# Optimization experiments

Measured on AMD Instinct MI355X. Metric: run time of the kernel, lower is better.

The kernel has to match this reference:

```python
import jax, jax.numpy as jnp
import numpy as np

NEG_SLOPE = 0.2  # PyG GATConv default negative_slope
BN_EPS = 1e-5


def gat_layer(x, src, dst, W, b, a_src, a_dst, heads, out_ch, concat):
    # x: [N, Fin]; W: [Fin, heads*out_ch]; a_src/a_dst: [heads, out_ch]
    N = x.shape[0]
    h = (x @ W).reshape(N, heads, out_ch)
    s = (h * a_src).sum(-1)            # [N, H]
    d = (h * a_dst).sum(-1)            # [N, H]
    e = jax.nn.leaky_relu(s[src] + d[dst], NEG_SLOPE)   # [E, H]
    # segment softmax over incoming edges of each destination node
    m = jax.ops.segment_max(e, dst, num_segments=N)
    ex = jnp.exp(e - m[dst])
    denom = jax.ops.segment_sum(ex, dst, num_segments=N)
    alpha = ex / (denom[dst] + 1e-16)                   # [E, H]
    out = jax.ops.segment_sum(alpha[:, :, None] * h[src], dst, num_segments=N)  # [N,H,C]
    out = out.reshape(N, heads * out_ch) if concat else out.mean(axis=1)
    return out + b


def batchnorm(x, gamma, beta):
    mu = x.mean(axis=0)
    var = x.var(axis=0)
    return gamma * (x - mu) * jax.lax.rsqrt(var + BN_EPS) + beta


def setup_inputs() -> dict:
    key = jax.random.key(0)
    ks = jax.random.split(key, 24)
    N, E, Fin, Hd, heads, C = 50000, 800000, 128, 64, 4, 2
    wdim = Hd * heads  # 256
    inp = {
        'x': jax.random.normal(ks[0], (N, Fin), jnp.float32),
        'edge_index': jax.random.randint(ks[1], (2, E), 0, N, jnp.int64),
    }
    def glorot(k, shape):
        fan = shape[0] + shape[-1]
        return jax.random.normal(k, shape, jnp.float32) * np.sqrt(2.0 / fan)
    # layer 0: Fin -> heads x Hd (concat)
    inp['W0'] = glorot(ks[2], (Fin, wdim)); inp['b0'] = jnp.zeros((wdim,), jnp.float32)
    inp['asrc0'] = glorot(ks[3], (heads, Hd)); inp['adst0'] = glorot(ks[4], (heads, Hd))
    inp['g0'] = jnp.ones((wdim,), jnp.float32); inp['be0'] = jnp.zeros((wdim,), jnp.float32)
    # layer 1: wdim -> heads x Hd (concat)
    inp['W1'] = glorot(ks[5], (wdim, wdim)); inp['b1'] = jnp.zeros((wdim,), jnp.float32)
    inp['asrc1'] = glorot(ks[6], (heads, Hd)); inp['adst1'] = glorot(ks[7], (heads, Hd))
    inp['g1'] = jnp.ones((wdim,), jnp.float32); inp['be1'] = jnp.zeros((wdim,), jnp.float32)
    # layer 2: wdim -> 1 head x Hd (no concat)
    inp['W2'] = glorot(ks[8], (wdim, Hd)); inp['b2'] = jnp.zeros((Hd,), jnp.float32)
    inp['asrc2'] = glorot(ks[9], (1, Hd)); inp['adst2'] = glorot(ks[10], (1, Hd))
    inp['g2'] = jnp.ones((Hd,), jnp.float32); inp['be2'] = jnp.zeros((Hd,), jnp.float32)
    # classifier: Linear(2*Hd, Hd) -> ReLU -> Linear(Hd, C)
    inp['Wc1'] = glorot(ks[11], (2 * Hd, Hd)); inp['bc1'] = jnp.zeros((Hd,), jnp.float32)
    inp['Wc2'] = glorot(ks[12], (Hd, C)); inp['bc2'] = jnp.zeros((C,), jnp.float32)
    return inp


def reference(x, edge_index, W0, b0, asrc0, adst0, g0, be0,
              W1, b1, asrc1, adst1, g1, be1,
              W2, b2, asrc2, adst2, g2, be2,
              Wc1, bc1, Wc2, bc2):
    N = x.shape[0]
    # add self-loops (PyG GATConv default)
    loops = jnp.arange(N, dtype=edge_index.dtype)
    src = jnp.concatenate([edge_index[0], loops])
    dst = jnp.concatenate([edge_index[1], loops])
    heads, Hd = asrc0.shape[0], asrc0.shape[1]

    h = gat_layer(x, src, dst, W0, b0, asrc0, adst0, heads, Hd, True)
    h = jax.nn.relu(batchnorm(h, g0, be0))
    h = gat_layer(h, src, dst, W1, b1, asrc1, adst1, heads, Hd, True)
    h = jax.nn.relu(batchnorm(h, g1, be1))
    h = gat_layer(h, src, dst, W2, b2, asrc2, adst2, 1, Hd, False)
    h = jax.nn.relu(batchnorm(h, g2, be2))

    pooled = jnp.concatenate([h.mean(axis=0, keepdims=True),
                              h.max(axis=0, keepdims=True)], axis=1)  # [1, 2*Hd]
    z = jax.nn.relu(pooled @ Wc1 + bc1)
    return z @ Wc2 + bc2  # [1, num_classes]
```

## Files before the change

### kernel.cpp

```cpp
#include <hip/hip_runtime.h>


typedef unsigned int uint;
typedef unsigned short ushort;

#define NEG_SLOPE 0.2f
#define BN_EPS 1e-5f
#define NB_RED 256

typedef __attribute__((ext_vector_type(2))) float f32x2;

__device__ __forceinline__ float bf2f(uint u) { return __uint_as_float(u << 16); }
__device__ __forceinline__ ushort f2bf(float f) {
    uint u = __float_as_uint(f);
    u += 0x7fff + ((u >> 16) & 1);
    return (ushort)(u >> 16);
}


__global__ void prep_kernel(const float* __restrict__ x, ushort* __restrict__ xb,
                            int total_real, int total_pad,
                            const float* __restrict__ W0, ushort* __restrict__ w0t,
                            const float* __restrict__ W1, ushort* __restrict__ w1t,
                            const float* __restrict__ W2, ushort* __restrict__ w2t,
                            const int* __restrict__ ei, int* __restrict__ deg, int E) {
    int i = blockIdx.x * blockDim.x + threadIdx.x;
    if (i < total_pad) {
        xb[i] = (i < total_real) ? f2bf(x[i]) : (ushort)0;
        return;
    }
    int j = i - total_pad;
    if (j < 32768) {
        int n = j / 128, k = j - n * 128;
        w0t[j] = f2bf(W0[(size_t)k * 256 + n]);
        return;
    }
    j -= 32768;
    if (j < 65536) {
        int n = j / 256, k = j - n * 256;
        w1t[j] = f2bf(W1[(size_t)k * 256 + n]);
        return;
    }
    j -= 65536;
    if (j < 16384) {
        int n = j / 256, k = j - n * 256;
        w2t[j] = f2bf(W2[(size_t)k * 64 + n]);
        return;
    }
    j -= 16384;
    if (j < E) atomicAdd(&deg[ei[E + j]], 1);
}


__global__ void scan_part(const int* __restrict__ deg, int* __restrict__ offsets,
                          int* __restrict__ bsum, int N) {
    __shared__ int sh[256];
    int t = threadIdx.x;
    int base = blockIdx.x * 1024 + t * 4;
    int v0 = (base + 0 < N) ? deg[base + 0] : 0;
    int v1 = (base + 1 < N) ? deg[base + 1] : 0;
    int v2 = (base + 2 < N) ? deg[base + 2] : 0;
    int v3 = (base + 3 < N) ? deg[base + 3] : 0;
    int s = v0 + v1 + v2 + v3;
    sh[t] = s;
    __syncthreads();
    for (int off = 1; off < 256; off <<= 1) {
        int y = (t >= off) ? sh[t - off] : 0;
        __syncthreads();
        sh[t] += y;
        __syncthreads();
    }
    int p = sh[t] - s;
    if (base + 0 < N) offsets[base + 0] = p;
    p += v0;
    if (base + 1 < N) offsets[base + 1] = p;
    p += v1;
    if (base + 2 < N) offsets[base + 2] = p;
    p += v2;
    if (base + 3 < N) offsets[base + 3] = p;
    if (t == 255) bsum[blockIdx.x] = sh[255];
}

__global__ void scan_top(const int* __restrict__ bsum, int* __restrict__ bexcl,
                         int nb, int* __restrict__ offsets, int N) {
    if (threadIdx.x == 0) {
        int run = 0;
        for (int b = 0; b < nb; ++b) { bexcl[b] = run; run += bsum[b]; }
        offsets[N] = run;
    }
}

__global__ void scan_add(int* __restrict__ offsets, int* __restrict__ cursor,
                         const int* __restrict__ bexcl, int N) {
    int add = bexcl[blockIdx.x];
    int base = blockIdx.x * 1024 + threadIdx.x * 4;
#pragma unroll
    for (int k = 0; k < 4; ++k) {
        int i = base + k;
        if (i < N) { int v = offsets[i] + add; offsets[i] = v; cursor[i] = v; }
    }
}

__global__ void scatter_kernel(const int* __restrict__ ei, int* __restrict__ cursor,
                               int* __restrict__ srcs, int E) {
    int e = blockIdx.x * blockDim.x + threadIdx.x;
    if (e < E) {
        int s = ei[e];
        int d = ei[E + e];
        int p = atomicAdd(&cursor[d], 1);
        srcs[p] = s;
    }
}


typedef __attribute__((ext_vector_type(8))) short bf16x8;
typedef __attribute__((ext_vector_type(4))) float floatx4;

template <int BN, int H>
__launch_bounds__(256)
__global__ void mfma_gemm_bt(const ushort* __restrict__ A, const ushort* __restrict__ Bt,
                             ushort* __restrict__ C, const float* __restrict__ asrc,
                             const float* __restrict__ adst, float* __restrict__ sv,
                             float* __restrict__ dv, int K, int Nn, int Mpad) {
    constexpr int WCOLS = (BN == 128) ? 2 : 1;
    constexpr int WROWS = 4 / WCOLS;
    constexpr int MT = 128 / (WROWS * 16);
    constexpr int NT = BN / (WCOLS * 16);
    constexpr int BCALLS = (BN * 32 * 2) / 4096;
    constexpr int SCH = (BN == 64) ? 8 : 32;
    constexpr int SSH = (BN == 64) ? 3 : 5;

    __shared__ ushort As[128 * 32];
    __shared__ ushort Bs[BN * 32];

    int t = threadIdx.x;
    int w = t >> 6, l = t & 63;

    int rb, cb;
    if (BN == 128) {
        int nbr = (int)gridDim.x >> 1;
        int full = (nbr & ~7) << 1;
        int id = blockIdx.x;
        if (id < full) {
            rb = ((id >> 4) << 3) + (id & 7);
            cb = (id >> 3) & 1;
        } else {
            int o = id - full;
            int rem = nbr & 7;
            rb = (nbr & ~7) + (rem ? (o % rem) : 0);
            cb = rem ? (o / rem) : 0;
        }
    } else {
        rb = blockIdx.x;
        cb = 0;
    }
    int row0 = rb * 128;
    int col0 = cb * BN;
    int wr = (w / WCOLS) * (MT * 16);
    int wc = (w % WCOLS) * (NT * 16);

    floatx4 acc[MT][NT];
#pragma unroll
    for (int mi = 0; mi < MT; ++mi)
#pragma unroll
        for (int ni = 0; ni < NT; ++ni)
#pragma unroll
            for (int r = 0; r < 4; ++r) acc[mi][ni][r] = 0.f;

    int mrow = l & 15;
    int kc = (l >> 4) * 8;

    for (int kt = 0; kt < K; kt += 32) {
#pragma unroll
        for (int c = 0; c < 2; ++c) {
            int idx = c * 256 + t;
            const ushort* gp = A + (size_t)(row0 + (idx >> 2)) * K + kt + (idx & 3) * 8;
            __builtin_amdgcn_global_load_lds(
                (const __attribute__((address_space(1))) void*)gp,
                (__attribute__((address_space(3))) void*)(As + (idx & ~63) * 8),
                16, 0, 0);
        }
#pragma unroll
        for (int c = 0; c < BCALLS; ++c) {
            int idx = c * 256 + t;
            const ushort* gp = Bt + (size_t)(col0 + (idx >> 2)) * K + kt + (idx & 3) * 8;
            __builtin_amdgcn_global_load_lds(
                (const __attribute__((address_space(1))) void*)gp,
                (__attribute__((address_space(3))) void*)(Bs + (idx & ~63) * 8),
                16, 0, 0);
        }
        __syncthreads();

        bf16x8 af[MT], bfr[NT];
#pragma unroll
        for (int mi = 0; mi < MT; ++mi)
            af[mi] = *(const bf16x8*)&As[(wr + mi * 16 + mrow) * 32 + kc];
#pragma unroll
        for (int ni = 0; ni < NT; ++ni)
            bfr[ni] = *(const bf16x8*)&Bs[(wc + ni * 16 + mrow) * 32 + kc];
#pragma unroll
        for (int mi = 0; mi < MT; ++mi)
#pragma unroll
            for (int ni = 0; ni < NT; ++ni)
                acc[mi][ni] = __builtin_amdgcn_mfma_f32_16x16x32_bf16(
                    af[mi], bfr[ni], acc[mi][ni], 0, 0, 0);
        __syncthreads();
    }

#pragma unroll
    for (int mi = 0; mi < MT; ++mi) {
        int rbase = row0 + wr + mi * 16 + (l >> 4) * 4;
#pragma unroll
        for (int ni = 0; ni < NT; ++ni) {
            int col = col0 + wc + ni * 16 + (l & 15);
            size_t sb = ((size_t)(col >> SSH) * Mpad) * SCH + (col & (SCH - 1));
#pragma unroll
            for (int r = 0; r < 4; ++r)
                C[sb + (size_t)(rbase + r) * SCH] = f2bf(acc[mi][ni][r]);
        }
    }

    float av[NT], bv[NT];
#pragma unroll
    for (int ni = 0; ni < NT; ++ni) {
        int ch = col0 + wc + ni * 16 + (l & 15);
        av[ni] = asrc[ch];
        bv[ni] = adst[ch];
    }
    int gh = (col0 + wc) >> 6;
#pragma unroll
    for (int mi = 0; mi < MT; ++mi) {
#pragma unroll
        for (int r = 0; r < 4; ++r) {
            float s = 0.f, d = 0.f;
#pragma unroll
            for (int ni = 0; ni < NT; ++ni) {
                float hv = acc[mi][ni][r];
                s += hv * av[ni];
                d += hv * bv[ni];
            }
#pragma unroll
            for (int m = 8; m >= 1; m >>= 1) {
                s += __shfl_xor(s, m);
                d += __shfl_xor(d, m);
            }
            if ((l & 15) == 0) {
                int row = row0 + wr + mi * 16 + (l >> 4) * 4 + r;
                sv[row * H + gh] = s;
                dv[row * H + gh] = d;
            }
        }
    }
}


#define CAP4 64

#define ACCUMW4(qv_, wt_) { \
    f32x2 wv_ = {(wt_), (wt_)}; \
    uint pr_[4] = {(qv_).x, (qv_).y, (qv_).z, (qv_).w}; \
    _Pragma("unroll") \
    for (int k_ = 0; k_ < 4; ++k_) { \
        f32x2 hv_ = {__uint_as_float(pr_[k_] << 16), \
                     __uint_as_float(pr_[k_] & 0xffff0000u)}; \
        ax[k_] += wv_ * hv_; \
    } }

#define LDQ4(kk_, wv_, qv_) { \
    int kq_ = (kk_); \
    if (kq_ < scnt) { \
        int nq_ = sidx[sub][kq_]; \
        wv_ = swgt[sub][kq_]; \
        qv_ = *(const uint4*)(gbase + (size_t)nq_ * 32); \
    } else { wv_ = 0.f; qv_.x = 0; qv_.y = 0; qv_.z = 0; qv_.w = 0; } }

__launch_bounds__(128)
__global__ void agg4_kernel(const ushort* __restrict__ hbT, const float* __restrict__ sv,
                            const float* __restrict__ dv, const int* __restrict__ offsets,
                            const int* __restrict__ srcs, const float* __restrict__ bias,
                            ushort* __restrict__ zb, int N, int Mpad) {
    __shared__ int   sidx[8][CAP4];
    __shared__ float swgt[8][CAP4];

    int t = threadIdx.x;
    int sub = t >> 4, gl = t & 15;
    int bid = blockIdx.x;
    int c = bid & 7;
    int head = c >> 1;
    int i = (bid >> 3) * 8 + sub;
    bool valid = i < N;

    int beg = 0, cnt = 0;
    if (valid) { beg = offsets[i]; cnt = offsets[i + 1] - beg; }
    int scnt = cnt < CAP4 ? cnt : CAP4;

    for (int k = gl; k < scnt; k += 16) sidx[sub][k] = srcs[beg + k];
    __syncthreads();

    float dvh = valid ? dv[i * 4 + head] : 0.f;
    float den = 0.f;
    for (int k = gl; k < scnt; k += 16) {
        float e = sv[sidx[sub][k] * 4 + head] + dvh;
        float wgt = __expf(fminf(fmaxf(e, NEG_SLOPE * e), 60.f));
        swgt[sub][k] = wgt;
        den += wgt;
    }
    den += __shfl_xor(den, 1);
    den += __shfl_xor(den, 2);
    den += __shfl_xor(den, 4);
    den += __shfl_xor(den, 8);
    __syncthreads();

    f32x2 ax[4] = {};
    int chunk = gl & 3;
    int esub = gl >> 2;
    const ushort* gbase = hbT + (size_t)c * Mpad * 32 + chunk * 8;

    float wA, wB;
    uint4 qA, qB;
    LDQ4(esub, wA, qA);
    LDQ4(esub + 4, wB, qB);
    for (int k = esub; k < scnt; k += 8) {
        float v0 = wA, v1 = wB;
        uint4 p0 = qA, p1 = qB;
        LDQ4(k + 8, wA, qA);
        LDQ4(k + 12, wB, qB);
        ACCUMW4(p0, v0);
        ACCUMW4(p1, v1);
    }

    if (cnt > CAP4) {
        float dslow = 0.f;
        for (int k2 = CAP4 + esub; k2 < cnt; k2 += 4) {
            int n = srcs[beg + k2];
            float e = sv[n * 4 + head] + dvh;
            float wgt = __expf(fminf(fmaxf(e, NEG_SLOPE * e), 60.f));
            if (chunk == 0) dslow += wgt;
            uint4 q4 = *(const uint4*)(gbase + (size_t)n * 32);
            ACCUMW4(q4, wgt);
        }
        dslow += __shfl_xor(dslow, 1);
        dslow += __shfl_xor(dslow, 2);
        dslow += __shfl_xor(dslow, 4);
        dslow += __shfl_xor(dslow, 8);
        den += dslow;
    }

#pragma unroll
    for (int j = 0; j < 4; ++j) {
        ax[j].x += __shfl_xor(ax[j].x, 4);
        ax[j].y += __shfl_xor(ax[j].y, 4);
        ax[j].x += __shfl_xor(ax[j].x, 8);
        ax[j].y += __shfl_xor(ax[j].y, 8);
    }

    if (valid && esub == 0) {
        float e_self = sv[i * 4 + head] + dvh;
        float wself = __expf(fminf(fmaxf(e_self, NEG_SLOPE * e_self), 60.f));
        uint4 qs = *(const uint4*)(gbase + (size_t)i * 32);
        ACCUMW4(qs, wself);
        float rden = 1.f / (den + wself + 1e-16f);
        const float* bb = bias + c * 32 + chunk * 8;
        uint4 o;
        o.x = (uint)f2bf(ax[0].x * rden + bb[0]) | ((uint)f2bf(ax[0].y * rden + bb[1]) << 16);
        o.y = (uint)f2bf(ax[1].x * rden + bb[2]) | ((uint)f2bf(ax[1].y * rden + bb[3]) << 16);
        o.z = (uint)f2bf(ax[2].x * rden + bb[4]) | ((uint)f2bf(ax[2].y * rden + bb[5]) << 16);
        o.w = (uint)f2bf(ax[3].x * rden + bb[6]) | ((uint)f2bf(ax[3].y * rden + bb[7]) << 16);
        *(uint4*)&zb[(size_t)i * 256 + c * 32 + chunk * 8] = o;
    }
}


__launch_bounds__(64)
__global__ void agg1_kernel(const ushort* __restrict__ hbT, const float* __restrict__ sv,
                            const float* __restrict__ dv, const int* __restrict__ offsets,
                            const int* __restrict__ srcs, const float* __restrict__ bias,
                            ushort* __restrict__ zb, int N, int Mpad) {
    int t = threadIdx.x;
    int sub = t >> 3, gl = t & 7;
    int bid = blockIdx.x;
    int c = bid & 7;
    int i = (bid >> 3) * 8 + sub;
    bool valid = i < N;

    int beg = 0, cnt = 0;
    if (valid) { beg = offsets[i]; cnt = offsets[i + 1] - beg; }

    float d_i = valid ? dv[i] : 0.f;
    const ushort* gbase = hbT + (size_t)c * Mpad * 8;

    f32x2 ax[4] = {};
    float den = 0.f;

    int k = gl;
    int nA = (k < cnt) ? srcs[beg + k] : 0;
    while (k < cnt) {
        int kn = k + 8;
        int nB = (kn < cnt) ? srcs[beg + kn] : 0;
        float s = sv[nA];
        uint4 q = *(const uint4*)(gbase + (size_t)nA * 8);
        float e = s + d_i;
        float wgt = __expf(fminf(fmaxf(e, NEG_SLOPE * e), 60.f));
        den += wgt;
        ACCUMW4(q, wgt);
        k = kn; nA = nB;
    }

    den += __shfl_xor(den, 1);
    den += __shfl_xor(den, 2);
    den += __shfl_xor(den, 4);
#pragma unroll
    for (int j = 0; j < 4; ++j) {
        ax[j].x += __shfl_xor(ax[j].x, 1);
        ax[j].y += __shfl_xor(ax[j].y, 1);
        ax[j].x += __shfl_xor(ax[j].x, 2);
        ax[j].y += __shfl_xor(ax[j].y, 2);
        ax[j].x += __shfl_xor(ax[j].x, 4);
        ax[j].y += __shfl_xor(ax[j].y, 4);
    }

    if (valid && gl == 0) {
        float e_self = sv[i] + d_i;
        float wself = __expf(fminf(fmaxf(e_self, NEG_SLOPE * e_self), 60.f));
        uint4 qs = *(const uint4*)(gbase + (size_t)i * 8);
        ACCUMW4(qs, wself);
        float rden = 1.f / (den + wself + 1e-16f);
        const float* bb = bias + c * 8;
        uint4 o;
        o.x = (uint)f2bf(ax[0].x * rden + bb[0]) | ((uint)f2bf(ax[0].y * rden + bb[1]) << 16);
        o.y = (uint)f2bf(ax[1].x * rden + bb[2]) | ((uint)f2bf(ax[1].y * rden + bb[3]) << 16);
        o.z = (uint)f2bf(ax[2].x * rden + bb[4]) | ((uint)f2bf(ax[2].y * rden + bb[5]) << 16);
        o.w = (uint)f2bf(ax[3].x * rden + bb[6]) | ((uint)f2bf(ax[3].y * rden + bb[7]) << 16);
        *(uint4*)&zb[(size_t)i * 64 + c * 8] = o;
    }
}


template <int F>
__launch_bounds__(256)
__global__ void bn_stats_kernel(const ushort* __restrict__ x, float* __restrict__ ps,
                                float* __restrict__ pq, int N) {
    constexpr int OCT = F / 8;
    __shared__ float lds_s[F], lds_q[F];
    int t = threadIdx.x;
    if (t < F) { lds_s[t] = 0.f; lds_q[t] = 0.f; }
    __syncthreads();

    float s[8] = {}, q[8] = {};
    int total8 = N * F / 8;
    for (int idx = blockIdx.x * 256 + t; idx < total8; idx += NB_RED * 256) {
        uint4 v = ((const uint4*)x)[idx];
        uint pr[4] = {v.x, v.y, v.z, v.w};
#pragma unroll
        for (int k = 0; k < 4; ++k) {
            float a = bf2f(pr[k] & 0xffffu);
            float b = bf2f(pr[k] >> 16);
            s[2 * k] += a;     q[2 * k] += a * a;
            s[2 * k + 1] += b; q[2 * k + 1] += b * b;
        }
    }
    int co = t % OCT;
#pragma unroll
    for (int j = 0; j < 8; ++j) {
        atomicAdd(&lds_s[co * 8 + j], s[j]);
        atomicAdd(&lds_q[co * 8 + j], q[j]);
    }
    __syncthreads();
    if (t < F) {
        ps[blockIdx.x * F + t] = lds_s[t];
        pq[blockIdx.x * F + t] = lds_q[t];
    }
}

__global__ void bn_final_kernel(const float* __restrict__ ps, const float* __restrict__ pq,
                                const float* __restrict__ g, const float* __restrict__ be,
                                float* __restrict__ scale, float* __restrict__ shift,
                                int N, int F) {
    int t = threadIdx.x;
    if (t < F) {
        float s = 0.f, q = 0.f;
        for (int b = 0; b < NB_RED; ++b) { s += ps[b * F + t]; q += pq[b * F + t]; }
        float mean = s / (float)N;
        float var = q / (float)N - mean * mean;
        float sc = g[t] * rsqrtf(var + BN_EPS);
        scale[t] = sc;
        shift[t] = be[t] - sc * mean;
    }
}

__global__ void bn_apply_kernel(uint* __restrict__ x, const float* __restrict__ scale,
                                const float* __restrict__ shift, int totalPairs, int Fmask) {
    int i = blockIdx.x * blockDim.x + threadIdx.x;
    if (i < totalPairs) {
        uint p = x[i];
        int c0 = (2 * i) & Fmask;
        float v0 = fmaxf(bf2f(p & 0xffffu) * scale[c0] + shift[c0], 0.f);
        float v1 = fmaxf(bf2f(p >> 16) * scale[c0 + 1] + shift[c0 + 1], 0.f);
        x[i] = (uint)f2bf(v0) | ((uint)f2bf(v1) << 16);
    }
}


__launch_bounds__(256)
__global__ void pool_kernel(const ushort* __restrict__ y, const float* __restrict__ scale,
                            const float* __restrict__ shift, float* __restrict__ psum,
                            float* __restrict__ pmax, int N) {
    constexpr int F = 64, OCT = 8;
    __shared__ float lds_s[F];
    __shared__ uint lds_m[F];
    int t = threadIdx.x;
    if (t < F) { lds_s[t] = 0.f; lds_m[t] = 0u; }
    __syncthreads();

    int co = t % OCT;
    float sc[8], sh[8];
#pragma unroll
    for (int j = 0; j < 8; ++j) { sc[j] = scale[co * 8 + j]; sh[j] = shift[co * 8 + j]; }

    float s[8] = {}, m[8] = {};
    int total8 = N * F / 8;
    for (int idx = blockIdx.x * 256 + t; idx < total8; idx += NB_RED * 256) {
        uint4 v = ((const uint4*)y)[idx];
        uint pr[4] = {v.x, v.y, v.z, v.w};
#pragma unroll
        for (int k = 0; k < 4; ++k) {
            float a = fmaxf(bf2f(pr[k] & 0xffffu) * sc[2 * k] + sh[2 * k], 0.f);
            float b = fmaxf(bf2f(pr[k] >> 16) * sc[2 * k + 1] + sh[2 * k + 1], 0.f);
            s[2 * k] += a;     m[2 * k] = fmaxf(m[2 * k], a);
            s[2 * k + 1] += b; m[2 * k + 1] = fmaxf(m[2 * k + 1], b);
        }
    }
#pragma unroll
    for (int j = 0; j < 8; ++j) {
        atomicAdd(&lds_s[co * 8 + j], s[j]);
        atomicMax(&lds_m[co * 8 + j], __float_as_uint(m[j]));
    }
    __syncthreads();
    if (t < F) {
        psum[blockIdx.x * F + t] = lds_s[t];
        pmax[blockIdx.x * F + t] = __uint_as_float(lds_m[t]);
    }
}

__global__ void classify_kernel(const float* __restrict__ psum, const float* __restrict__ pmax,
                                const float* __restrict__ Wc1, const float* __restrict__ bc1,
                                const float* __restrict__ Wc2, const float* __restrict__ bc2,
                                float* __restrict__ out, int N) {
    __shared__ float pooled[128];
    __shared__ float z[64];
    int t = threadIdx.x;
    if (t < 64) {
        float s = 0.f;
        for (int b = 0; b < NB_RED; ++b) s += psum[b * 64 + t];
        pooled[t] = s / (float)N;
    } else {
        int c = t - 64;
        float m = 0.f;
        for (int b = 0; b < NB_RED; ++b) m = fmaxf(m, pmax[b * 64 + c]);
        pooled[t] = m;
    }
    __syncthreads();
    if (t < 64) {
        float a = bc1[t];
        for (int k = 0; k < 128; ++k) a += pooled[k] * Wc1[k * 64 + t];
        z[t] = a > 0.f ? a : 0.f;
    }
    __syncthreads();
    if (t < 2) {
        float a = bc2[t];
        for (int j = 0; j < 64; ++j) a += z[j] * Wc2[j * 2 + t];
        out[t] = a;
    }
}


extern "C" void kernel_launch(void* const* d_in, const int* in_sizes, int n_in,
                              void* d_out, int out_size, void* d_ws, size_t ws_size,
                              hipStream_t stream) {
    const float* x   = (const float*)d_in[0];
    const int*   ei  = (const int*)d_in[1];
    const float* W0  = (const float*)d_in[2];  const float* b0  = (const float*)d_in[3];
    const float* as0 = (const float*)d_in[4];  const float* ad0 = (const float*)d_in[5];
    const float* g0  = (const float*)d_in[6];  const float* be0 = (const float*)d_in[7];
    const float* W1  = (const float*)d_in[8];  const float* b1  = (const float*)d_in[9];
    const float* as1 = (const float*)d_in[10]; const float* ad1 = (const float*)d_in[11];
    const float* g1  = (const float*)d_in[12]; const float* be1 = (const float*)d_in[13];
    const float* W2  = (const float*)d_in[14]; const float* b2  = (const float*)d_in[15];
    const float* as2 = (const float*)d_in[16]; const float* ad2 = (const float*)d_in[17];
    const float* g2  = (const float*)d_in[18]; const float* be2 = (const float*)d_in[19];
    const float* Wc1 = (const float*)d_in[20]; const float* bc1 = (const float*)d_in[21];
    const float* Wc2 = (const float*)d_in[22]; const float* bc2 = (const float*)d_in[23];
    float* out = (float*)d_out;

    const int N = in_sizes[0] / 128;
    const int E = in_sizes[1] / 2;
    const int Mpad = ((N + 127) / 128) * 128;
    const int NB_SCAN = (N + 1023) / 1024;
    const int NBROW = Mpad / 128;
    const int NB_AGG = ((N + 7) / 8) * 8;

    char* ws = (char*)d_ws;
    size_t o = 0;
    auto alloc = [&](size_t bytes) -> void* {
        void* p = ws + o;
        o = (o + bytes + 255) & ~(size_t)255;
        return p;
    };
    int*    deg     = (int*)alloc((size_t)N * 4);
    int*    offsets = (int*)alloc((size_t)(N + 1) * 4);
    int*    cursor  = (int*)alloc((size_t)N * 4);
    int*    srcs    = (int*)alloc((size_t)E * 4);
    int*    bsum    = (int*)alloc((size_t)NB_SCAN * 4);
    int*    bexcl   = (int*)alloc((size_t)NB_SCAN * 4);
    ushort* xb      = (ushort*)alloc((size_t)Mpad * 128 * 2);
    ushort* w0t     = (ushort*)alloc((size_t)256 * 128 * 2);
    ushort* w1t     = (ushort*)alloc((size_t)256 * 256 * 2);
    ushort* w2t     = (ushort*)alloc((size_t)64 * 256 * 2);
    ushort* hb      = (ushort*)alloc((size_t)Mpad * 256 * 2);
    ushort* zb      = (ushort*)alloc((size_t)Mpad * 256 * 2);
    float*  sv      = (float*)alloc((size_t)Mpad * 4 * 4);
    float*  dv      = (float*)alloc((size_t)Mpad * 4 * 4);
    float*  ps      = (float*)alloc((size_t)NB_RED * 256 * 4);
    float*  pq      = (float*)alloc((size_t)NB_RED * 256 * 4);
    float*  scale   = (float*)alloc(256 * 4);
    float*  shift   = (float*)alloc(256 * 4);
    float*  psum    = (float*)alloc((size_t)NB_RED * 64 * 4);
    float*  pmax    = (float*)alloc((size_t)NB_RED * 64 * 4);

    (void)hipMemsetAsync(deg, 0, (size_t)N * 4, stream);
    int prep_total = Mpad * 128 + 32768 + 65536 + 16384 + E;
    prep_kernel<<<(prep_total + 255) / 256, 256, 0, stream>>>(
        x, xb, N * 128, Mpad * 128, W0, w0t, W1, w1t, W2, w2t, ei, deg, E);

    scan_part<<<NB_SCAN, 256, 0, stream>>>(deg, offsets, bsum, N);
    scan_top<<<1, 64, 0, stream>>>(bsum, bexcl, NB_SCAN, offsets, N);
    scan_add<<<NB_SCAN, 256, 0, stream>>>(offsets, cursor, bexcl, N);
    scatter_kernel<<<(E + 255) / 256, 256, 0, stream>>>(ei, cursor, srcs, E);

    {
        mfma_gemm_bt<128, 4><<<NBROW * 2, 256, 0, stream>>>(xb, w0t, hb, as0, ad0, sv, dv,
                                                            128, 256, Mpad);
        agg4_kernel<<<NB_AGG, 128, 0, stream>>>(hb, sv, dv, offsets, srcs, b0, zb, N, Mpad);
        bn_stats_kernel<256><<<NB_RED, 256, 0, stream>>>(zb, ps, pq, N);
        bn_final_kernel<<<1, 256, 0, stream>>>(ps, pq, g0, be0, scale, shift, N, 256);
        bn_apply_kernel<<<(N * 128 + 255) / 256, 256, 0, stream>>>((uint*)zb, scale, shift,
                                                                   N * 128, 255);
    }
    {
        mfma_gemm_bt<128, 4><<<NBROW * 2, 256, 0, stream>>>(zb, w1t, hb, as1, ad1, sv, dv,
                                                            256, 256, Mpad);
        agg4_kernel<<<NB_AGG, 128, 0, stream>>>(hb, sv, dv, offsets, srcs, b1, zb, N, Mpad);
        bn_stats_kernel<256><<<NB_RED, 256, 0, stream>>>(zb, ps, pq, N);
        bn_final_kernel<<<1, 256, 0, stream>>>(ps, pq, g1, be1, scale, shift, N, 256);
        bn_apply_kernel<<<(N * 128 + 255) / 256, 256, 0, stream>>>((uint*)zb, scale, shift,
                                                                   N * 128, 255);
    }
    {
        mfma_gemm_bt<64, 1><<<NBROW, 256, 0, stream>>>(zb, w2t, hb, as2, ad2, sv, dv,
                                                       256, 64, Mpad);
        agg1_kernel<<<NB_AGG, 64, 0, stream>>>(hb, sv, dv, offsets, srcs, b2, zb, N, Mpad);
        bn_stats_kernel<64><<<NB_RED, 256, 0, stream>>>(zb, ps, pq, N);
        bn_final_kernel<<<1, 64, 0, stream>>>(ps, pq, g2, be2, scale, shift, N, 64);
    }

    pool_kernel<<<NB_RED, 256, 0, stream>>>(zb, scale, shift, psum, pmax, N);
    classify_kernel<<<1, 128, 0, stream>>>(psum, pmax, Wc1, bc1, Wc2, bc2, out, N);
}
```

Baseline: 651.6 us.

## Precompute per-edge attention weights in separate kernel before aggregation

Adds wgt4/wgt1 kernels that compute each edge's exp-leakyrelu attention weight and per-node denominator once, storing (src, weight) pairs per head. The aggregation kernels then read these packed pairs instead of recomputing weights in each of the 8 column-chunk blocks, which also removes the shared-memory staging, syncthreads and the high-degree slow path. The cost is an extra launch per layer and writing then reading 4*E*8 bytes of pair data through global memory.

```diff
diff --git a/kernel.cpp b/kernel.cpp
--- a/kernel.cpp
+++ b/kernel.cpp
@@ -254,7 +254,59 @@
 }
 
 
-#define CAP4 64
+__launch_bounds__(128)
+__global__ void wgt4_kernel(const float* __restrict__ sv, const float* __restrict__ dv,
+                            const int* __restrict__ offsets, const int* __restrict__ srcs,
+                            uint2* __restrict__ pw4, float* __restrict__ den4,
+                            int N, int E) {
+    int t = threadIdx.x;
+    int sub = t >> 4, gl = t & 15;
+    int head = gl >> 2, eo = gl & 3;
+    int i = blockIdx.x * 8 + sub;
+    if (i >= N) return;
+    int beg = offsets[i], cnt = offsets[i + 1] - beg;
+    float dvh = dv[i * 4 + head];
+    float den = 0.f;
+    uint2* pwh = pw4 + (size_t)head * E + beg;
+    for (int k = eo; k < cnt; k += 4) {
+        int src = srcs[beg + k];
+        float e = sv[src * 4 + head] + dvh;
+        float w = __expf(fminf(fmaxf(e, NEG_SLOPE * e), 60.f));
+        uint2 pv; pv.x = (uint)src; pv.y = __float_as_uint(w);
+        pwh[k] = pv;
+        den += w;
+    }
+    den += __shfl_xor(den, 1);
+    den += __shfl_xor(den, 2);
+    if (eo == 0) den4[i * 4 + head] = den;
+}
+
+
+__launch_bounds__(64)
+__global__ void wgt1_kernel(const float* __restrict__ sv, const float* __restrict__ dv,
+                            const int* __restrict__ offsets, const int* __restrict__ srcs,
+                            uint2* __restrict__ pw1, float* __restrict__ den1, int N) {
+    int t = threadIdx.x;
+    int sub = t >> 3, gl = t & 7;
+    int i = blockIdx.x * 8 + sub;
+    if (i >= N) return;
+    int beg = offsets[i], cnt = offsets[i + 1] - beg;
+    float d_i = dv[i];
+    float den = 0.f;
+    for (int k = gl; k < cnt; k += 8) {
+        int src = srcs[beg + k];
+        float e = sv[src] + d_i;
+        float w = __expf(fminf(fmaxf(e, NEG_SLOPE * e), 60.f));
+        uint2 pv; pv.x = (uint)src; pv.y = __float_as_uint(w);
+        pw1[beg + k] = pv;
+        den += w;
+    }
+    den += __shfl_xor(den, 1);
+    den += __shfl_xor(den, 2);
+    den += __shfl_xor(den, 4);
+    if (gl == 0) den1[i] = den;
+}
+
 
 #define ACCUMW4(qv_, wt_) { \
     f32x2 wv_ = {(wt_), (wt_)}; \
@@ -266,84 +318,37 @@
         ax[k_] += wv_ * hv_; \
     } }
 
-#define LDQ4(kk_, wv_, qv_) { \
-    int kq_ = (kk_); \
-    if (kq_ < scnt) { \
-        int nq_ = sidx[sub][kq_]; \
-        wv_ = swgt[sub][kq_]; \
-        qv_ = *(const uint4*)(gbase + (size_t)nq_ * 32); \
-    } else { wv_ = 0.f; qv_.x = 0; qv_.y = 0; qv_.z = 0; qv_.w = 0; } }
-
 __launch_bounds__(128)
 __global__ void agg4_kernel(const ushort* __restrict__ hbT, const float* __restrict__ sv,
                             const float* __restrict__ dv, const int* __restrict__ offsets,
-                            const int* __restrict__ srcs, const float* __restrict__ bias,
-                            ushort* __restrict__ zb, int N, int Mpad) {
-    __shared__ int   sidx[8][CAP4];
-    __shared__ float swgt[8][CAP4];
-
+                            const uint2* __restrict__ pw4, const float* __restrict__ den4,
+                            const float* __restrict__ bias, ushort* __restrict__ zb,
+                            int N, int Mpad, int E) {
     int t = threadIdx.x;
     int sub = t >> 4, gl = t & 15;
     int bid = blockIdx.x;
     int c = bid & 7;
     int head = c >> 1;
     int i = (bid >> 3) * 8 + sub;
-    bool valid = i < N;
-
-    int beg = 0, cnt = 0;
-    if (valid) { beg = offsets[i]; cnt = offsets[i + 1] - beg; }
-    int scnt = cnt < CAP4 ? cnt : CAP4;
-
-    for (int k = gl; k < scnt; k += 16) sidx[sub][k] = srcs[beg + k];
-    __syncthreads();
-
-    float dvh = valid ? dv[i * 4 + head] : 0.f;
-    float den = 0.f;
-    for (int k = gl; k < scnt; k += 16) {
-        float e = sv[sidx[sub][k] * 4 + head] + dvh;
-        float wgt = __expf(fminf(fmaxf(e, NEG_SLOPE * e), 60.f));
-        swgt[sub][k] = wgt;
-        den += wgt;
-    }
-    den += __shfl_xor(den, 1);
-    den += __shfl_xor(den, 2);
-    den += __shfl_xor(den, 4);
-    den += __shfl_xor(den, 8);
-    __syncthreads();
+    if (i >= N) return;
+
+    int beg = offsets[i], cnt = offsets[i + 1] - beg;
+    int chunk = gl & 3, esub = gl >> 2;
+    const ushort* gbase = hbT + (size_t)c * Mpad * 32 + chunk * 8;
+    const uint2* pwh = pw4 + (size_t)head * E + beg;
 
     f32x2 ax[4] = {};
-    int chunk = gl & 3;
-    int esub = gl >> 2;
-    const ushort* gbase = hbT + (size_t)c * Mpad * 32 + chunk * 8;
-
-    float wA, wB;
-    uint4 qA, qB;
-    LDQ4(esub, wA, qA);
-    LDQ4(esub + 4, wB, qB);
-    for (int k = esub; k < scnt; k += 8) {
-        float v0 = wA, v1 = wB;
-        uint4 p0 = qA, p1 = qB;
-        LDQ4(k + 8, wA, qA);
-        LDQ4(k + 12, wB, qB);
-        ACCUMW4(p0, v0);
-        ACCUMW4(p1, v1);
-    }
-
-    if (cnt > CAP4) {
-        float dslow = 0.f;
-        for (int k2 = CAP4 + esub; k2 < cnt; k2 += 4) {
-            int n = srcs[beg + k2];
-            float e = sv[n * 4 + head] + dvh;
-            float wgt = __expf(fminf(fmaxf(e, NEG_SLOPE * e), 60.f));
-            if (chunk == 0) dslow += wgt;
-            uint4 q4 = *(const uint4*)(gbase + (size_t)n * 32);
-            ACCUMW4(q4, wgt);
-        }
-        dslow += __shfl_xor(dslow, 1);
-        dslow += __shfl_xor(dslow, 2);
-        dslow += __shfl_xor(dslow, 4);
-        dslow += __shfl_xor(dslow, 8);
-        den += dslow;
+    int k = esub;
+    uint2 pA; pA.x = 0u; pA.y = 0u;
+    if (k < cnt) pA = pwh[k];
+    while (k < cnt) {
+        int kn = k + 4;
+        uint2 pB; pB.x = 0u; pB.y = 0u;
+        if (kn < cnt) pB = pwh[kn];
+        uint4 q = *(const uint4*)(gbase + (size_t)pA.x * 32);
+        float w = __uint_as_float(pA.y);
+        ACCUMW4(q, w);
+        k = kn; pA = pB;
     }
 
 #pragma unroll
@@ -354,12 +359,13 @@
         ax[j].y += __shfl_xor(ax[j].y, 8);
     }
 
-    if (valid && esub == 0) {
+    if (esub == 0) {
+        float dvh = dv[i * 4 + head];
         float e_self = sv[i * 4 + head] + dvh;
         float wself = __expf(fminf(fmaxf(e_self, NEG_SLOPE * e_self), 60.f));
         uint4 qs = *(const uint4*)(gbase + (size_t)i * 32);
         ACCUMW4(qs, wself);
-        float rden = 1.f / (den + wself + 1e-16f);
+        float rden = 1.f / (den4[i * 4 + head] + wself + 1e-16f);
         const float* bb = bias + c * 32 + chunk * 8;
         uint4 o;
         o.x = (uint)f2bf(ax[0].x * rden + bb[0]) | ((uint)f2bf(ax[0].y * rden + bb[1]) << 16);
@@ -374,41 +380,34 @@
 __launch_bounds__(64)
 __global__ void agg1_kernel(const ushort* __restrict__ hbT, const float* __restrict__ sv,
                             const float* __restrict__ dv, const int* __restrict__ offsets,
-                            const int* __restrict__ srcs, const float* __restrict__ bias,
-                            ushort* __restrict__ zb, int N, int Mpad) {
+                            const uint2* __restrict__ pw1, const float* __restrict__ den1,
+                            const float* __restrict__ bias, ushort* __restrict__ zb,
+                            int N, int Mpad) {
     int t = threadIdx.x;
     int sub = t >> 3, gl = t & 7;
     int bid = blockIdx.x;
     int c = bid & 7;
     int i = (bid >> 3) * 8 + sub;
-    bool valid = i < N;
-
-    int beg = 0, cnt = 0;
-    if (valid) { beg = offsets[i]; cnt = offsets[i + 1] - beg; }
-
-    float d_i = valid ? dv[i] : 0.f;
+    if (i >= N) return;
+
+    int beg = offsets[i], cnt = offsets[i + 1] - beg;
     const ushort* gbase = hbT + (size_t)c * Mpad * 8;
+    const uint2* pw = pw1 + beg;
 
     f32x2 ax[4] = {};
-    float den = 0.f;
-
     int k = gl;
-    int nA = (k < cnt) ? srcs[beg + k] : 0;
+    uint2 pA; pA.x = 0u; pA.y = 0u;
+    if (k < cnt) pA = pw[k];
     while (k < cnt) {
         int kn = k + 8;
-        int nB = (kn < cnt) ? srcs[beg + kn] : 0;
-        float s = sv[nA];
-        uint4 q = *(const uint4*)(gbase + (size_t)nA * 8);
-        float e = s + d_i;
-        float wgt = __expf(fminf(fmaxf(e, NEG_SLOPE * e), 60.f));
-        den += wgt;
-        ACCUMW4(q, wgt);
-        k = kn; nA = nB;
-    }
-
-    den += __shfl_xor(den, 1);
-    den += __shfl_xor(den, 2);
-    den += __shfl_xor(den, 4);
+        uint2 pB; pB.x = 0u; pB.y = 0u;
+        if (kn < cnt) pB = pw[kn];
+        uint4 q = *(const uint4*)(gbase + (size_t)pA.x * 8);
+        float w = __uint_as_float(pA.y);
+        ACCUMW4(q, w);
+        k = kn; pA = pB;
+    }
+
 #pragma unroll
     for (int j = 0; j < 4; ++j) {
         ax[j].x += __shfl_xor(ax[j].x, 1);
@@ -419,12 +418,13 @@
         ax[j].y += __shfl_xor(ax[j].y, 4);
     }
 
-    if (valid && gl == 0) {
+    if (gl == 0) {
+        float d_i = dv[i];
         float e_self = sv[i] + d_i;
         float wself = __expf(fminf(fmaxf(e_self, NEG_SLOPE * e_self), 60.f));
         uint4 qs = *(const uint4*)(gbase + (size_t)i * 8);
         ACCUMW4(qs, wself);
-        float rden = 1.f / (den + wself + 1e-16f);
+        float rden = 1.f / (den1[i] + wself + 1e-16f);
         const float* bb = bias + c * 8;
         uint4 o;
         o.x = (uint)f2bf(ax[0].x * rden + bb[0]) | ((uint)f2bf(ax[0].y * rden + bb[1]) << 16);
@@ -597,7 +597,8 @@
     const int Mpad = ((N + 127) / 128) * 128;
     const int NB_SCAN = (N + 1023) / 1024;
     const int NBROW = Mpad / 128;
-    const int NB_AGG = ((N + 7) / 8) * 8;
+    const int NB_N8  = (N + 7) / 8;
+    const int NB_AGG = NB_N8 * 8;
 
     char* ws = (char*)d_ws;
     size_t o = 0;
@@ -620,6 +621,10 @@
     ushort* zb      = (ushort*)alloc((size_t)Mpad * 256 * 2);
     float*  sv      = (float*)alloc((size_t)Mpad * 4 * 4);
     float*  dv      = (float*)alloc((size_t)Mpad * 4 * 4);
+    uint2*  pw4     = (uint2*)alloc((size_t)4 * E * 8);
+    uint2*  pw1     = (uint2*)alloc((size_t)E * 8);
+    float*  den4    = (float*)alloc((size_t)Mpad * 4 * 4);
+    float*  den1    = (float*)alloc((size_t)Mpad * 4);
     float*  ps      = (float*)alloc((size_t)NB_RED * 256 * 4);
     float*  pq      = (float*)alloc((size_t)NB_RED * 256 * 4);
     float*  scale   = (float*)alloc(256 * 4);
@@ -640,7 +645,9 @@
     {
         mfma_gemm_bt<128, 4><<<NBROW * 2, 256, 0, stream>>>(xb, w0t, hb, as0, ad0, sv, dv,
                                                             128, 256, Mpad);
-        agg4_kernel<<<NB_AGG, 128, 0, stream>>>(hb, sv, dv, offsets, srcs, b0, zb, N, Mpad);
+        wgt4_kernel<<<NB_N8, 128, 0, stream>>>(sv, dv, offsets, srcs, pw4, den4, N, E);
+        agg4_kernel<<<NB_AGG, 128, 0, stream>>>(hb, sv, dv, offsets, pw4, den4, b0, zb,
+                                                N, Mpad, E);
         bn_stats_kernel<256><<<NB_RED, 256, 0, stream>>>(zb, ps, pq, N);
         bn_final_kernel<<<1, 256, 0, stream>>>(ps, pq, g0, be0, scale, shift, N, 256);
         bn_apply_kernel<<<(N * 128 + 255) / 256, 256, 0, stream>>>((uint*)zb, scale, shift,
@@ -649,7 +656,9 @@
     {
         mfma_gemm_bt<128, 4><<<NBROW * 2, 256, 0, stream>>>(zb, w1t, hb, as1, ad1, sv, dv,
                                                             256, 256, Mpad);
-        agg4_kernel<<<NB_AGG, 128, 0, stream>>>(hb, sv, dv, offsets, srcs, b1, zb, N, Mpad);
+        wgt4_kernel<<<NB_N8, 128, 0, stream>>>(sv, dv, offsets, srcs, pw4, den4, N, E);
+        agg4_kernel<<<NB_AGG, 128, 0, stream>>>(hb, sv, dv, offsets, pw4, den4, b1, zb,
+                                                N, Mpad, E);
         bn_stats_kernel<256><<<NB_RED, 256, 0, stream>>>(zb, ps, pq, N);
         bn_final_kernel<<<1, 256, 0, stream>>>(ps, pq, g1, be1, scale, shift, N, 256);
         bn_apply_kernel<<<(N * 128 + 255) / 256, 256, 0, stream>>>((uint*)zb, scale, shift,
@@ -658,7 +667,9 @@
     {
         mfma_gemm_bt<64, 1><<<NBROW, 256, 0, stream>>>(zb, w2t, hb, as2, ad2, sv, dv,
                                                        256, 64, Mpad);
-        agg1_kernel<<<NB_AGG, 64, 0, stream>>>(hb, sv, dv, offsets, srcs, b2, zb, N, Mpad);
+        wgt1_kernel<<<NB_N8, 64, 0, stream>>>(sv, dv, offsets, srcs, pw1, den1, N);
+        agg1_kernel<<<NB_AGG, 64, 0, stream>>>(hb, sv, dv, offsets, pw1, den1, b2, zb,
+                                               N, Mpad);
         bn_stats_kernel<64><<<NB_RED, 256, 0, stream>>>(zb, ps, pq, N);
         bn_final_kernel<<<1, 64, 0, stream>>>(ps, pq, g2, be2, scale, shift, N, 64);
     }
```

New measurement: 640.2 us. About the same (-1.8%).

## Map one thread per node-chunk in GAT aggregation, dropping shared staging

Applied to the files above, without the earlier changes.

Both aggregation kernels are restructured so each thread walks a destination node's whole edge list serially for its feature chunk. Previously a group of 16 or 8 lanes split the edges, staged indices and weights in shared memory, and reduced with shuffles. The change removes shared-memory staging, block barriers and cross-lane reductions, and grows blocks to 256 threads over more nodes. In exchange, latency is hidden only by one-ahead prefetching within a thread. Threads in a wave now have uneven trip counts that track node degree, and each edge is visited by four chunk threads instead of sixteen sharing the work.

```diff
diff --git a/kernel.cpp b/kernel.cpp
--- a/kernel.cpp
+++ b/kernel.cpp
@@ -254,8 +254,6 @@
 }
 
 
-#define CAP4 64
-
 #define ACCUMW4(qv_, wt_) { \
     f32x2 wv_ = {(wt_), (wt_)}; \
     uint pr_[4] = {(qv_).x, (qv_).y, (qv_).z, (qv_).w}; \
@@ -266,173 +264,114 @@
         ax[k_] += wv_ * hv_; \
     } }
 
-#define LDQ4(kk_, wv_, qv_) { \
-    int kq_ = (kk_); \
-    if (kq_ < scnt) { \
-        int nq_ = sidx[sub][kq_]; \
-        wv_ = swgt[sub][kq_]; \
-        qv_ = *(const uint4*)(gbase + (size_t)nq_ * 32); \
-    } else { wv_ = 0.f; qv_.x = 0; qv_.y = 0; qv_.z = 0; qv_.w = 0; } }
-
-__launch_bounds__(128)
+__launch_bounds__(256)
 __global__ void agg4_kernel(const ushort* __restrict__ hbT, const float* __restrict__ sv,
                             const float* __restrict__ dv, const int* __restrict__ offsets,
                             const int* __restrict__ srcs, const float* __restrict__ bias,
                             ushort* __restrict__ zb, int N, int Mpad) {
-    __shared__ int   sidx[8][CAP4];
-    __shared__ float swgt[8][CAP4];
-
-    int t = threadIdx.x;
-    int sub = t >> 4, gl = t & 15;
+    int t = threadIdx.x;
+    int nlocal = t >> 2, chunk = t & 3;
     int bid = blockIdx.x;
     int c = bid & 7;
     int head = c >> 1;
-    int i = (bid >> 3) * 8 + sub;
-    bool valid = i < N;
-
-    int beg = 0, cnt = 0;
-    if (valid) { beg = offsets[i]; cnt = offsets[i + 1] - beg; }
-    int scnt = cnt < CAP4 ? cnt : CAP4;
-
-    for (int k = gl; k < scnt; k += 16) sidx[sub][k] = srcs[beg + k];
-    __syncthreads();
-
-    float dvh = valid ? dv[i * 4 + head] : 0.f;
+    int i = (bid >> 3) * 64 + nlocal;
+    if (i >= N) return;
+
+    int beg = offsets[i], end = offsets[i + 1];
+    float dvh = dv[i * 4 + head];
+    const ushort* gbase = hbT + (size_t)c * Mpad * 32 + chunk * 8;
+
+    f32x2 ax[4] = {};
     float den = 0.f;
-    for (int k = gl; k < scnt; k += 16) {
-        float e = sv[sidx[sub][k] * 4 + head] + dvh;
+
+    int k = beg;
+    int sA = 0; float vA = 0.f; uint4 qA; qA.x = 0u; qA.y = 0u; qA.z = 0u; qA.w = 0u;
+    if (k < end) {
+        sA = srcs[k];
+        vA = sv[sA * 4 + head];
+        qA = *(const uint4*)(gbase + (size_t)sA * 32);
+    }
+    while (k < end) {
+        int kn = k + 1;
+        int sB = 0; float vB = 0.f; uint4 qB; qB.x = 0u; qB.y = 0u; qB.z = 0u; qB.w = 0u;
+        if (kn < end) {
+            sB = srcs[kn];
+            vB = sv[sB * 4 + head];
+            qB = *(const uint4*)(gbase + (size_t)sB * 32);
+        }
+        float e = vA + dvh;
         float wgt = __expf(fminf(fmaxf(e, NEG_SLOPE * e), 60.f));
-        swgt[sub][k] = wgt;
         den += wgt;
-    }
-    den += __shfl_xor(den, 1);
-    den += __shfl_xor(den, 2);
-    den += __shfl_xor(den, 4);
-    den += __shfl_xor(den, 8);
-    __syncthreads();
-
-    f32x2 ax[4] = {};
-    int chunk = gl & 3;
-    int esub = gl >> 2;
-    const ushort* gbase = hbT + (size_t)c * Mpad * 32 + chunk * 8;
-
-    float wA, wB;
-    uint4 qA, qB;
-    LDQ4(esub, wA, qA);
-    LDQ4(esub + 4, wB, qB);
-    for (int k = esub; k < scnt; k += 8) {
-        float v0 = wA, v1 = wB;
-        uint4 p0 = qA, p1 = qB;
-        LDQ4(k + 8, wA, qA);
-        LDQ4(k + 12, wB, qB);
-        ACCUMW4(p0, v0);
-        ACCUMW4(p1, v1);
-    }
-
-    if (cnt > CAP4) {
-        float dslow = 0.f;
-        for (int k2 = CAP4 + esub; k2 < cnt; k2 += 4) {
-            int n = srcs[beg + k2];
-            float e = sv[n * 4 + head] + dvh;
-            float wgt = __expf(fminf(fmaxf(e, NEG_SLOPE * e), 60.f));
-            if (chunk == 0) dslow += wgt;
-            uint4 q4 = *(const uint4*)(gbase + (size_t)n * 32);
-            ACCUMW4(q4, wgt);
-        }
-        dslow += __shfl_xor(dslow, 1);
-        dslow += __shfl_xor(dslow, 2);
-        dslow += __shfl_xor(dslow, 4);
-        dslow += __shfl_xor(dslow, 8);
-        den += dslow;
-    }
-
-#pragma unroll
-    for (int j = 0; j < 4; ++j) {
-        ax[j].x += __shfl_xor(ax[j].x, 4);
-        ax[j].y += __shfl_xor(ax[j].y, 4);
-        ax[j].x += __shfl_xor(ax[j].x, 8);
-        ax[j].y += __shfl_xor(ax[j].y, 8);
-    }
-
-    if (valid && esub == 0) {
-        float e_self = sv[i * 4 + head] + dvh;
-        float wself = __expf(fminf(fmaxf(e_self, NEG_SLOPE * e_self), 60.f));
-        uint4 qs = *(const uint4*)(gbase + (size_t)i * 32);
-        ACCUMW4(qs, wself);
-        float rden = 1.f / (den + wself + 1e-16f);
-        const float* bb = bias + c * 32 + chunk * 8;
-        uint4 o;
-        o.x = (uint)f2bf(ax[0].x * rden + bb[0]) | ((uint)f2bf(ax[0].y * rden + bb[1]) << 16);
-        o.y = (uint)f2bf(ax[1].x * rden + bb[2]) | ((uint)f2bf(ax[1].y * rden + bb[3]) << 16);
-        o.z = (uint)f2bf(ax[2].x * rden + bb[4]) | ((uint)f2bf(ax[2].y * rden + bb[5]) << 16);
-        o.w = (uint)f2bf(ax[3].x * rden + bb[6]) | ((uint)f2bf(ax[3].y * rden + bb[7]) << 16);
-        *(uint4*)&zb[(size_t)i * 256 + c * 32 + chunk * 8] = o;
-    }
-}
-
-
-__launch_bounds__(64)
+        ACCUMW4(qA, wgt);
+        k = kn; sA = sB; vA = vB; qA = qB;
+    }
+
+    float e_self = sv[i * 4 + head] + dvh;
+    float wself = __expf(fminf(fmaxf(e_self, NEG_SLOPE * e_self), 60.f));
+    uint4 qs = *(const uint4*)(gbase + (size_t)i * 32);
+    ACCUMW4(qs, wself);
+    float rden = 1.f / (den + wself + 1e-16f);
+    const float* bb = bias + c * 32 + chunk * 8;
+    uint4 o;
+    o.x = (uint)f2bf(ax[0].x * rden + bb[0]) | ((uint)f2bf(ax[0].y * rden + bb[1]) << 16);
+    o.y = (uint)f2bf(ax[1].x * rden + bb[2]) | ((uint)f2bf(ax[1].y * rden + bb[3]) << 16);
+    o.z = (uint)f2bf(ax[2].x * rden + bb[4]) | ((uint)f2bf(ax[2].y * rden + bb[5]) << 16);
+    o.w = (uint)f2bf(ax[3].x * rden + bb[6]) | ((uint)f2bf(ax[3].y * rden + bb[7]) << 16);
+    *(uint4*)&zb[(size_t)i * 256 + c * 32 + chunk * 8] = o;
+}
+
+__launch_bounds__(256)
 __global__ void agg1_kernel(const ushort* __restrict__ hbT, const float* __restrict__ sv,
                             const float* __restrict__ dv, const int* __restrict__ offsets,
                             const int* __restrict__ srcs, const float* __restrict__ bias,
                             ushort* __restrict__ zb, int N, int Mpad) {
     int t = threadIdx.x;
-    int sub = t >> 3, gl = t & 7;
     int bid = blockIdx.x;
     int c = bid & 7;
-    int i = (bid >> 3) * 8 + sub;
-    bool valid = i < N;
-
-    int beg = 0, cnt = 0;
-    if (valid) { beg = offsets[i]; cnt = offsets[i + 1] - beg; }
-
-    float d_i = valid ? dv[i] : 0.f;
+    int i = (bid >> 3) * 256 + t;
+    if (i >= N) return;
+
+    int beg = offsets[i], end = offsets[i + 1];
+    float d_i = dv[i];
     const ushort* gbase = hbT + (size_t)c * Mpad * 8;
 
     f32x2 ax[4] = {};
     float den = 0.f;
 
-    int k = gl;
-    int nA = (k < cnt) ? srcs[beg + k] : 0;
-    while (k < cnt) {
-        int kn = k + 8;
-        int nB = (kn < cnt) ? srcs[beg + kn] : 0;
-        float s = sv[nA];
-        uint4 q = *(const uint4*)(gbase + (size_t)nA * 8);
-        float e = s + d_i;
+    int k = beg;
+    int sA = 0; float vA = 0.f; uint4 qA; qA.x = 0u; qA.y = 0u; qA.z = 0u; qA.w = 0u;
+    if (k < end) {
+        sA = srcs[k];
+        vA = sv[sA];
+        qA = *(const uint4*)(gbase + (size_t)sA * 8);
+    }
+    while (k < end) {
+        int kn = k + 1;
+        int sB = 0; float vB = 0.f; uint4 qB; qB.x = 0u; qB.y = 0u; qB.z = 0u; qB.w = 0u;
+        if (kn < end) {
+            sB = srcs[kn];
+            vB = sv[sB];
+            qB = *(const uint4*)(gbase + (size_t)sB * 8);
+        }
+        float e = vA + d_i;
         float wgt = __expf(fminf(fmaxf(e, NEG_SLOPE * e), 60.f));
         den += wgt;
-        ACCUMW4(q, wgt);
-        k = kn; nA = nB;
-    }
-
-    den += __shfl_xor(den, 1);
-    den += __shfl_xor(den, 2);
-    den += __shfl_xor(den, 4);
-#pragma unroll
-    for (int j = 0; j < 4; ++j) {
-        ax[j].x += __shfl_xor(ax[j].x, 1);
-        ax[j].y += __shfl_xor(ax[j].y, 1);
-        ax[j].x += __shfl_xor(ax[j].x, 2);
-        ax[j].y += __shfl_xor(ax[j].y, 2);
-        ax[j].x += __shfl_xor(ax[j].x, 4);
-        ax[j].y += __shfl_xor(ax[j].y, 4);
-    }
-
-    if (valid && gl == 0) {
-        float e_self = sv[i] + d_i;
-        float wself = __expf(fminf(fmaxf(e_self, NEG_SLOPE * e_self), 60.f));
-        uint4 qs = *(const uint4*)(gbase + (size_t)i * 8);
-        ACCUMW4(qs, wself);
-        float rden = 1.f / (den + wself + 1e-16f);
-        const float* bb = bias + c * 8;
-        uint4 o;
-        o.x = (uint)f2bf(ax[0].x * rden + bb[0]) | ((uint)f2bf(ax[0].y * rden + bb[1]) << 16);
-        o.y = (uint)f2bf(ax[1].x * rden + bb[2]) | ((uint)f2bf(ax[1].y * rden + bb[3]) << 16);
-        o.z = (uint)f2bf(ax[2].x * rden + bb[4]) | ((uint)f2bf(ax[2].y * rden + bb[5]) << 16);
-        o.w = (uint)f2bf(ax[3].x * rden + bb[6]) | ((uint)f2bf(ax[3].y * rden + bb[7]) << 16);
-        *(uint4*)&zb[(size_t)i * 64 + c * 8] = o;
-    }
+        ACCUMW4(qA, wgt);
+        k = kn; sA = sB; vA = vB; qA = qB;
+    }
+
+    float e_self = sv[i] + d_i;
+    float wself = __expf(fminf(fmaxf(e_self, NEG_SLOPE * e_self), 60.f));
+    uint4 qs = *(const uint4*)(gbase + (size_t)i * 8);
+    ACCUMW4(qs, wself);
+    float rden = 1.f / (den + wself + 1e-16f);
+    const float* bb = bias + c * 8;
+    uint4 o;
+    o.x = (uint)f2bf(ax[0].x * rden + bb[0]) | ((uint)f2bf(ax[0].y * rden + bb[1]) << 16);
+    o.y = (uint)f2bf(ax[1].x * rden + bb[2]) | ((uint)f2bf(ax[1].y * rden + bb[3]) << 16);
+    o.z = (uint)f2bf(ax[2].x * rden + bb[4]) | ((uint)f2bf(ax[2].y * rden + bb[5]) << 16);
+    o.w = (uint)f2bf(ax[3].x * rden + bb[6]) | ((uint)f2bf(ax[3].y * rden + bb[7]) << 16);
+    *(uint4*)&zb[(size_t)i * 64 + c * 8] = o;
 }
 
 
@@ -597,7 +536,8 @@
     const int Mpad = ((N + 127) / 128) * 128;
     const int NB_SCAN = (N + 1023) / 1024;
     const int NBROW = Mpad / 128;
-    const int NB_AGG = ((N + 7) / 8) * 8;
+    const int NB_A4 = ((N + 63) / 64) * 8;
+    const int NB_A1 = ((N + 255) / 256) * 8;
 
     char* ws = (char*)d_ws;
     size_t o = 0;
@@ -640,7 +580,7 @@
     {
         mfma_gemm_bt<128, 4><<<NBROW * 2, 256, 0, stream>>>(xb, w0t, hb, as0, ad0, sv, dv,
                                                             128, 256, Mpad);
-        agg4_kernel<<<NB_AGG, 128, 0, stream>>>(hb, sv, dv, offsets, srcs, b0, zb, N, Mpad);
+        agg4_kernel<<<NB_A4, 256, 0, stream>>>(hb, sv, dv, offsets, srcs, b0, zb, N, Mpad);
         bn_stats_kernel<256><<<NB_RED, 256, 0, stream>>>(zb, ps, pq, N);
         bn_final_kernel<<<1, 256, 0, stream>>>(ps, pq, g0, be0, scale, shift, N, 256);
         bn_apply_kernel<<<(N * 128 + 255) / 256, 256, 0, stream>>>((uint*)zb, scale, shift,
@@ -649,7 +589,7 @@
     {
         mfma_gemm_bt<128, 4><<<NBROW * 2, 256, 0, stream>>>(zb, w1t, hb, as1, ad1, sv, dv,
                                                             256, 256, Mpad);
-        agg4_kernel<<<NB_AGG, 128, 0, stream>>>(hb, sv, dv, offsets, srcs, b1, zb, N, Mpad);
+        agg4_kernel<<<NB_A4, 256, 0, stream>>>(hb, sv, dv, offsets, srcs, b1, zb, N, Mpad);
         bn_stats_kernel<256><<<NB_RED, 256, 0, stream>>>(zb, ps, pq, N);
         bn_final_kernel<<<1, 256, 0, stream>>>(ps, pq, g1, be1, scale, shift, N, 256);
         bn_apply_kernel<<<(N * 128 + 255) / 256, 256, 0, stream>>>((uint*)zb, scale, shift,
@@ -658,7 +598,7 @@
     {
         mfma_gemm_bt<64, 1><<<NBROW, 256, 0, stream>>>(zb, w2t, hb, as2, ad2, sv, dv,
                                                        256, 64, Mpad);
-        agg1_kernel<<<NB_AGG, 64, 0, stream>>>(hb, sv, dv, offsets, srcs, b2, zb, N, Mpad);
+        agg1_kernel<<<NB_A1, 256, 0, stream>>>(hb, sv, dv, offsets, srcs, b2, zb, N, Mpad);
         bn_stats_kernel<64><<<NB_RED, 256, 0, stream>>>(zb, ps, pq, N);
         bn_final_kernel<<<1, 64, 0, stream>>>(ps, pq, g2, be2, scale, shift, N, 64);
     }
```

New measurement: 715.5 us. +9.8%, slower.
